# Optimization experiments

Hardware: AMD Instinct MI355X
Metric: run time of the kernel (lower is better)

## Reference

```python
import jax, jax.numpy as jnp
import numpy as np

SHAPE = (4096, 11008)


def setup_inputs() -> dict:
    key = jax.random.key(0)
    k1, k2, k3 = jax.random.split(key, 3)
    x = jax.random.normal(k1, SHAPE, dtype=jnp.float32)
    magnitude = jax.random.uniform(k2, SHAPE, dtype=jnp.float32)  # EMA state (non-negative)
    sparsity = jax.random.uniform(k3, (1,), dtype=jnp.float32)
    mask = jnp.ones(SHAPE, dtype=bool)
    t = 1  # step counter (self.t) as python int
    return {"x": x, "magnitude": magnitude, "sparsity": sparsity, "mask": mask, "t": t}


def reference(x, magnitude, sparsity, mask, t):
    # update_magnitude: EMA of |x| (done under no_grad in torch)
    t_f = jnp.float32(t)
    mag = (t_f * magnitude + jnp.abs(x)) / (t_f + 1.0)
    # prune_and_update_mask: sort-based k-th smallest magnitude threshold
    values = jnp.sort(mag.ravel())
    n = values.shape[0]
    # torch: idx = max(int(sparsity * n - 1), 0)
    idx = jnp.clip(jnp.floor(sparsity * n - 1.0).astype(jnp.int32), 0, n - 1)
    threshold = values[idx]  # shape (1,), broadcasts
    new_mask = mag >= threshold
    # broadcast_mul
    return x * new_mask.astype(x.dtype)
```

## Files before the change

kernel.cpp:

```cpp
#include <hip/hip_runtime.h>
#include <stdint.h>


#define LO_BITS 17
#define NB_HI   (1 << (32 - LO_BITS))
#define NB_LO   (1 << LO_BITS)

__device__ __forceinline__ uint32_t fkey(float f) {
    uint32_t u = __float_as_uint(f);
    return (u & 0x80000000u) ? ~u : (u | 0x80000000u);
}

__device__ __forceinline__ float magf(float x, float g, float tf, float den) {
    return (tf * g + fabsf(x)) / den;
}

__global__ __launch_bounds__(1024) void hist_hi_kernel(
    const float* __restrict__ x, const float* __restrict__ g,
    const int* __restrict__ tptr, uint32_t* __restrict__ hist_hi, int n)
{
    __shared__ uint32_t lh[NB_HI / 2];
    for (int i = threadIdx.x; i < NB_HI / 2; i += blockDim.x) lh[i] = 0;
    __syncthreads();
    const float tf  = (float)tptr[0];
    const float den = tf + 1.0f;
    const int n4 = n >> 2;
    const float4* x4 = (const float4*)x;
    const float4* g4 = (const float4*)g;
    const int gid = blockIdx.x * blockDim.x + threadIdx.x;
    const int stride = gridDim.x * blockDim.x;
    for (int i = gid; i < n4; i += stride) {
        float4 xv = x4[i], gv = g4[i];
        uint32_t b0 = fkey(magf(xv.x, gv.x, tf, den)) >> LO_BITS;
        uint32_t b1 = fkey(magf(xv.y, gv.y, tf, den)) >> LO_BITS;
        uint32_t b2 = fkey(magf(xv.z, gv.z, tf, den)) >> LO_BITS;
        uint32_t b3 = fkey(magf(xv.w, gv.w, tf, den)) >> LO_BITS;
        atomicAdd(&lh[b0 >> 1], 1u << ((b0 & 1) * 16));
        atomicAdd(&lh[b1 >> 1], 1u << ((b1 & 1) * 16));
        atomicAdd(&lh[b2 >> 1], 1u << ((b2 & 1) * 16));
        atomicAdd(&lh[b3 >> 1], 1u << ((b3 & 1) * 16));
    }
    for (int i = (n4 << 2) + gid; i < n; i += stride) {
        uint32_t b = fkey(magf(x[i], g[i], tf, den)) >> LO_BITS;
        atomicAdd(&lh[b >> 1], 1u << ((b & 1) * 16));
    }
    __syncthreads();
    for (int i = threadIdx.x; i < NB_HI / 2; i += blockDim.x) {
        uint32_t v = lh[i];
        uint32_t lo = v & 0xffffu, hi = v >> 16;
        if (lo) atomicAdd(&hist_hi[2 * i],     lo);
        if (hi) atomicAdd(&hist_hi[2 * i + 1], hi);
    }
}

__global__ __launch_bounds__(1024) void scan_kernel(
    const uint32_t* __restrict__ hist, uint32_t* __restrict__ ctl,
    const float* __restrict__ sparsity, int nbins, int phase, int n)
{
    const int tid = threadIdx.x;
    const int bpt = nbins >> 10;
    uint32_t kk;
    if (phase == 0) {
        float s = sparsity[0];
        float v = floorf(s * (float)n - 1.0f);
        long long idx = (long long)v;
        if (idx < 0) idx = 0;
        if (idx > (long long)(n - 1)) idx = n - 1;
        kk = (uint32_t)(idx + 1);
    } else {
        kk = ctl[1];
    }
    const int base = tid * bpt;
    uint32_t s = 0;
    for (int j = 0; j < bpt; ++j) s += hist[base + j];
    __shared__ uint32_t tmp[1024];
    tmp[tid] = s;
    __syncthreads();
    for (int off = 1; off < 1024; off <<= 1) {
        uint32_t v = (tid >= off) ? tmp[tid - off] : 0u;
        __syncthreads();
        tmp[tid] += v;
        __syncthreads();
    }
    const uint32_t incl = tmp[tid];
    const uint32_t excl = incl - s;
    if (excl < kk && incl >= kk) {
        uint32_t running = excl;
        for (int j = 0; j < bpt; ++j) {
            uint32_t c = hist[base + j];
            if (running + c >= kk) {
                uint32_t bin = (uint32_t)(base + j);
                if (phase == 0) { ctl[0] = bin; ctl[1] = kk - running; }
                else            { ctl[2] = (ctl[0] << LO_BITS) | bin; }
                break;
            }
            running += c;
        }
    }
}

__global__ __launch_bounds__(512) void hist_lo_kernel(
    const float* __restrict__ x, const float* __restrict__ g,
    const int* __restrict__ tptr, const uint32_t* __restrict__ ctl,
    uint32_t* __restrict__ hist_lo, int n)
{
    const uint32_t b   = ctl[0];
    const float tf  = (float)tptr[0];
    const float den = tf + 1.0f;
    const int n4 = n >> 2;
    const float4* x4 = (const float4*)x;
    const float4* g4 = (const float4*)g;
    const int gid = blockIdx.x * blockDim.x + threadIdx.x;
    const int stride = gridDim.x * blockDim.x;
    for (int i = gid; i < n4; i += stride) {
        float4 xv = x4[i], gv = g4[i];
        uint32_t k0 = fkey(magf(xv.x, gv.x, tf, den));
        uint32_t k1 = fkey(magf(xv.y, gv.y, tf, den));
        uint32_t k2 = fkey(magf(xv.z, gv.z, tf, den));
        uint32_t k3 = fkey(magf(xv.w, gv.w, tf, den));
        if ((k0 >> LO_BITS) == b) atomicAdd(&hist_lo[k0 & (NB_LO - 1)], 1u);
        if ((k1 >> LO_BITS) == b) atomicAdd(&hist_lo[k1 & (NB_LO - 1)], 1u);
        if ((k2 >> LO_BITS) == b) atomicAdd(&hist_lo[k2 & (NB_LO - 1)], 1u);
        if ((k3 >> LO_BITS) == b) atomicAdd(&hist_lo[k3 & (NB_LO - 1)], 1u);
    }
    for (int i = (n4 << 2) + gid; i < n; i += stride) {
        uint32_t k = fkey(magf(x[i], g[i], tf, den));
        if ((k >> LO_BITS) == b) atomicAdd(&hist_lo[k & (NB_LO - 1)], 1u);
    }
}

__global__ __launch_bounds__(512) void apply_kernel(
    const float* __restrict__ x, const float* __restrict__ g,
    const int* __restrict__ tptr, const uint32_t* __restrict__ ctl,
    float* __restrict__ out, int n)
{
    const uint32_t K = ctl[2];
    const float tf  = (float)tptr[0];
    const float den = tf + 1.0f;
    const int n4 = n >> 2;
    const float4* x4 = (const float4*)x;
    const float4* g4 = (const float4*)g;
    float4* o4 = (float4*)out;
    const int gid = blockIdx.x * blockDim.x + threadIdx.x;
    const int stride = gridDim.x * blockDim.x;
    for (int i = gid; i < n4; i += stride) {
        float4 xv = x4[i], gv = g4[i];
        float4 o;
        o.x = xv.x * ((fkey(magf(xv.x, gv.x, tf, den)) >= K) ? 1.0f : 0.0f);
        o.y = xv.y * ((fkey(magf(xv.y, gv.y, tf, den)) >= K) ? 1.0f : 0.0f);
        o.z = xv.z * ((fkey(magf(xv.z, gv.z, tf, den)) >= K) ? 1.0f : 0.0f);
        o.w = xv.w * ((fkey(magf(xv.w, gv.w, tf, den)) >= K) ? 1.0f : 0.0f);
        o4[i] = o;
    }
    for (int i = (n4 << 2) + gid; i < n; i += stride) {
        out[i] = x[i] * ((fkey(magf(x[i], g[i], tf, den)) >= K) ? 1.0f : 0.0f);
    }
}

extern "C" void kernel_launch(void* const* d_in, const int* in_sizes, int n_in,
                              void* d_out, int out_size, void* d_ws, size_t ws_size,
                              hipStream_t stream)
{
    const float* x  = (const float*)d_in[0];
    const float* g  = (const float*)d_in[1];
    const float* sp = (const float*)d_in[2];
    const int*   t  = (const int*)d_in[4];
    float* out = (float*)d_out;
    const int n = in_sizes[0];

    uint32_t* hist_hi = (uint32_t*)d_ws;
    uint32_t* hist_lo = hist_hi + NB_HI;
    uint32_t* ctl     = hist_lo + NB_LO;

    hipMemsetAsync(d_ws, 0, (size_t)(NB_HI + NB_LO + 3) * sizeof(uint32_t), stream);
    hist_hi_kernel<<<1024, 1024, 0, stream>>>(x, g, t, hist_hi, n);
    scan_kernel<<<1, 1024, 0, stream>>>(hist_hi, ctl, sp, NB_HI, 0, n);
    hist_lo_kernel<<<2048, 512, 0, stream>>>(x, g, t, ctl, hist_lo, n);
    scan_kernel<<<1, 1024, 0, stream>>>(hist_lo, ctl, sp, NB_LO, 1, n);
    apply_kernel<<<2048, 512, 0, stream>>>(x, g, t, ctl, out, n);
}
```

Measured before the change: 679.9 us.

## Parallelize histogram scan into segment sums and unroll streaming kernels with batched loads

Replaces the single-block prefix scan over each histogram with a multi-block segment-sum pass followed by a single block that scans only the chosen segment, so the serial scan over 128K bins is spread across many blocks. The three streaming kernels switch from grid-stride loops to one tile per block, with eight float4 loads per thread issued before any compute to raise memory-level parallelism. This adds two extra kernel launches and a fixed-size grid tied to n, and increases register pressure.

```diff
diff --git a/kernel.cpp b/kernel.cpp
--- a/kernel.cpp
+++ b/kernel.cpp
@@ -5,12 +5,12 @@
 #define LO_BITS 17
 #define NB_HI   (1 << (32 - LO_BITS))
 #define NB_LO   (1 << LO_BITS)
+#define NSEG    64
 
 __device__ __forceinline__ uint32_t fkey(float f) {
     uint32_t u = __float_as_uint(f);
     return (u & 0x80000000u) ? ~u : (u | 0x80000000u);
 }
-
 __device__ __forceinline__ float magf(float x, float g, float tf, float den) {
     return (tf * g + fabsf(x)) / den;
 }
@@ -20,32 +20,43 @@
     const int* __restrict__ tptr, uint32_t* __restrict__ hist_hi, int n)
 {
     __shared__ uint32_t lh[NB_HI / 2];
-    for (int i = threadIdx.x; i < NB_HI / 2; i += blockDim.x) lh[i] = 0;
+    for (int i = threadIdx.x; i < NB_HI / 2; i += 1024) lh[i] = 0;
     __syncthreads();
     const float tf  = (float)tptr[0];
     const float den = tf + 1.0f;
     const int n4 = n >> 2;
     const float4* x4 = (const float4*)x;
     const float4* g4 = (const float4*)g;
-    const int gid = blockIdx.x * blockDim.x + threadIdx.x;
-    const int stride = gridDim.x * blockDim.x;
-    for (int i = gid; i < n4; i += stride) {
-        float4 xv = x4[i], gv = g4[i];
-        uint32_t b0 = fkey(magf(xv.x, gv.x, tf, den)) >> LO_BITS;
-        uint32_t b1 = fkey(magf(xv.y, gv.y, tf, den)) >> LO_BITS;
-        uint32_t b2 = fkey(magf(xv.z, gv.z, tf, den)) >> LO_BITS;
-        uint32_t b3 = fkey(magf(xv.w, gv.w, tf, den)) >> LO_BITS;
-        atomicAdd(&lh[b0 >> 1], 1u << ((b0 & 1) * 16));
-        atomicAdd(&lh[b1 >> 1], 1u << ((b1 & 1) * 16));
-        atomicAdd(&lh[b2 >> 1], 1u << ((b2 & 1) * 16));
-        atomicAdd(&lh[b3 >> 1], 1u << ((b3 & 1) * 16));
-    }
-    for (int i = (n4 << 2) + gid; i < n; i += stride) {
-        uint32_t b = fkey(magf(x[i], g[i], tf, den)) >> LO_BITS;
-        atomicAdd(&lh[b >> 1], 1u << ((b & 1) * 16));
-    }
-    __syncthreads();
-    for (int i = threadIdx.x; i < NB_HI / 2; i += blockDim.x) {
+    const int base = blockIdx.x * 8192 + threadIdx.x;
+
+    float4 xv[8], gv[8];
+    #pragma unroll
+    for (int u = 0; u < 8; ++u) {
+        const int idx = base + u * 1024;
+        if (idx < n4) { xv[u] = x4[idx]; gv[u] = g4[idx]; }
+    }
+    #pragma unroll
+    for (int u = 0; u < 8; ++u) {
+        const int idx = base + u * 1024;
+        if (idx < n4) {
+            uint32_t b0 = fkey(magf(xv[u].x, gv[u].x, tf, den)) >> LO_BITS;
+            uint32_t b1 = fkey(magf(xv[u].y, gv[u].y, tf, den)) >> LO_BITS;
+            uint32_t b2 = fkey(magf(xv[u].z, gv[u].z, tf, den)) >> LO_BITS;
+            uint32_t b3 = fkey(magf(xv[u].w, gv[u].w, tf, den)) >> LO_BITS;
+            atomicAdd(&lh[b0 >> 1], 1u << ((b0 & 1) * 16));
+            atomicAdd(&lh[b1 >> 1], 1u << ((b1 & 1) * 16));
+            atomicAdd(&lh[b2 >> 1], 1u << ((b2 & 1) * 16));
+            atomicAdd(&lh[b3 >> 1], 1u << ((b3 & 1) * 16));
+        }
+    }
+    if (blockIdx.x == 0) {
+        for (int i = (n4 << 2) + threadIdx.x; i < n; i += 1024) {
+            uint32_t b = fkey(magf(x[i], g[i], tf, den)) >> LO_BITS;
+            atomicAdd(&lh[b >> 1], 1u << ((b & 1) * 16));
+        }
+    }
+    __syncthreads();
+    for (int i = threadIdx.x; i < NB_HI / 2; i += 1024) {
         uint32_t v = lh[i];
         uint32_t lo = v & 0xffffu, hi = v >> 16;
         if (lo) atomicAdd(&hist_hi[2 * i],     lo);
@@ -53,53 +64,95 @@
     }
 }
 
-__global__ __launch_bounds__(1024) void scan_kernel(
-    const uint32_t* __restrict__ hist, uint32_t* __restrict__ ctl,
-    const float* __restrict__ sparsity, int nbins, int phase, int n)
-{
+__global__ __launch_bounds__(256) void seg_kernel(
+    const uint32_t* __restrict__ hist, uint32_t* __restrict__ segsum, int bps)
+{
+    __shared__ uint32_t red[256];
+    const int base = blockIdx.x * bps;
+    uint32_t s = 0;
+    for (int j = threadIdx.x; j < bps; j += 256) s += hist[base + j];
+    red[threadIdx.x] = s;
+    __syncthreads();
+    for (int off = 128; off > 0; off >>= 1) {
+        if (threadIdx.x < off) red[threadIdx.x] += red[threadIdx.x + off];
+        __syncthreads();
+    }
+    if (threadIdx.x == 0) segsum[blockIdx.x] = red[0];
+}
+
+__global__ __launch_bounds__(1024) void find_kernel(
+    const uint32_t* __restrict__ hist, const uint32_t* __restrict__ segsum,
+    uint32_t* __restrict__ ctl, const float* __restrict__ sparsity,
+    int nbins, int phase, int n)
+{
+    const int bps = nbins / NSEG;
+    __shared__ uint32_t sseg[NSEG];
+    __shared__ uint32_t bins[2048];
+    __shared__ uint32_t scanbuf[1024];
+    __shared__ uint32_t skk, sseg_id;
     const int tid = threadIdx.x;
-    const int bpt = nbins >> 10;
-    uint32_t kk;
-    if (phase == 0) {
-        float s = sparsity[0];
-        float v = floorf(s * (float)n - 1.0f);
-        long long idx = (long long)v;
-        if (idx < 0) idx = 0;
-        if (idx > (long long)(n - 1)) idx = n - 1;
-        kk = (uint32_t)(idx + 1);
-    } else {
-        kk = ctl[1];
-    }
-    const int base = tid * bpt;
+    if (tid < NSEG) sseg[tid] = segsum[tid];
+    __syncthreads();
+    if (tid == 0) {
+        uint32_t kk;
+        if (phase == 0) {
+            float s = sparsity[0];
+            float v = floorf(s * (float)n - 1.0f);
+            long long idx = (long long)v;
+            if (idx < 0) idx = 0;
+            if (idx > (long long)(n - 1)) idx = n - 1;
+            kk = (uint32_t)(idx + 1);
+        } else {
+            kk = ctl[1];
+        }
+        uint32_t run = 0; uint32_t seg = NSEG - 1;
+        for (int j = 0; j < NSEG; ++j) {
+            if (run + sseg[j] >= kk) { seg = (uint32_t)j; break; }
+            run += sseg[j];
+        }
+        skk = kk - run;
+        sseg_id = seg;
+    }
+    __syncthreads();
+    const uint32_t kk = skk;
+    const int seg = (int)sseg_id;
+    for (int j = tid; j < bps; j += 1024) bins[j] = hist[seg * bps + j];
+    __syncthreads();
+    const int c = (bps + 1023) >> 10;
     uint32_t s = 0;
-    for (int j = 0; j < bpt; ++j) s += hist[base + j];
-    __shared__ uint32_t tmp[1024];
-    tmp[tid] = s;
+    for (int j = 0; j < c; ++j) {
+        int b0 = tid * c + j;
+        if (b0 < bps) s += bins[b0];
+    }
+    scanbuf[tid] = s;
     __syncthreads();
     for (int off = 1; off < 1024; off <<= 1) {
-        uint32_t v = (tid >= off) ? tmp[tid - off] : 0u;
+        uint32_t v = (tid >= off) ? scanbuf[tid - off] : 0u;
         __syncthreads();
-        tmp[tid] += v;
+        scanbuf[tid] += v;
         __syncthreads();
     }
-    const uint32_t incl = tmp[tid];
+    const uint32_t incl = scanbuf[tid];
     const uint32_t excl = incl - s;
     if (excl < kk && incl >= kk) {
-        uint32_t running = excl;
-        for (int j = 0; j < bpt; ++j) {
-            uint32_t c = hist[base + j];
-            if (running + c >= kk) {
-                uint32_t bin = (uint32_t)(base + j);
-                if (phase == 0) { ctl[0] = bin; ctl[1] = kk - running; }
-                else            { ctl[2] = (ctl[0] << LO_BITS) | bin; }
-                break;
+        uint32_t run = excl;
+        for (int j = 0; j < c; ++j) {
+            int b0 = tid * c + j;
+            if (b0 < bps) {
+                uint32_t cc = bins[b0];
+                if (run + cc >= kk) {
+                    uint32_t bin = (uint32_t)(seg * bps + b0);
+                    if (phase == 0) { ctl[0] = bin; ctl[1] = kk - run; }
+                    else            { ctl[2] = (ctl[0] << LO_BITS) | bin; }
+                    break;
+                }
+                run += cc;
             }
-            running += c;
-        }
-    }
-}
-
-__global__ __launch_bounds__(512) void hist_lo_kernel(
+        }
+    }
+}
+
+__global__ __launch_bounds__(256) void hist_lo_kernel(
     const float* __restrict__ x, const float* __restrict__ g,
     const int* __restrict__ tptr, const uint32_t* __restrict__ ctl,
     uint32_t* __restrict__ hist_lo, int n)
@@ -110,26 +163,37 @@
     const int n4 = n >> 2;
     const float4* x4 = (const float4*)x;
     const float4* g4 = (const float4*)g;
-    const int gid = blockIdx.x * blockDim.x + threadIdx.x;
-    const int stride = gridDim.x * blockDim.x;
-    for (int i = gid; i < n4; i += stride) {
-        float4 xv = x4[i], gv = g4[i];
-        uint32_t k0 = fkey(magf(xv.x, gv.x, tf, den));
-        uint32_t k1 = fkey(magf(xv.y, gv.y, tf, den));
-        uint32_t k2 = fkey(magf(xv.z, gv.z, tf, den));
-        uint32_t k3 = fkey(magf(xv.w, gv.w, tf, den));
-        if ((k0 >> LO_BITS) == b) atomicAdd(&hist_lo[k0 & (NB_LO - 1)], 1u);
-        if ((k1 >> LO_BITS) == b) atomicAdd(&hist_lo[k1 & (NB_LO - 1)], 1u);
-        if ((k2 >> LO_BITS) == b) atomicAdd(&hist_lo[k2 & (NB_LO - 1)], 1u);
-        if ((k3 >> LO_BITS) == b) atomicAdd(&hist_lo[k3 & (NB_LO - 1)], 1u);
-    }
-    for (int i = (n4 << 2) + gid; i < n; i += stride) {
-        uint32_t k = fkey(magf(x[i], g[i], tf, den));
-        if ((k >> LO_BITS) == b) atomicAdd(&hist_lo[k & (NB_LO - 1)], 1u);
-    }
-}
-
-__global__ __launch_bounds__(512) void apply_kernel(
+    const int base = blockIdx.x * 2048 + threadIdx.x;
+
+    float4 xv[8], gv[8];
+    #pragma unroll
+    for (int u = 0; u < 8; ++u) {
+        const int idx = base + u * 256;
+        if (idx < n4) { xv[u] = x4[idx]; gv[u] = g4[idx]; }
+    }
+    #pragma unroll
+    for (int u = 0; u < 8; ++u) {
+        const int idx = base + u * 256;
+        if (idx < n4) {
+            uint32_t k0 = fkey(magf(xv[u].x, gv[u].x, tf, den));
+            uint32_t k1 = fkey(magf(xv[u].y, gv[u].y, tf, den));
+            uint32_t k2 = fkey(magf(xv[u].z, gv[u].z, tf, den));
+            uint32_t k3 = fkey(magf(xv[u].w, gv[u].w, tf, den));
+            if ((k0 >> LO_BITS) == b) atomicAdd(&hist_lo[k0 & (NB_LO - 1)], 1u);
+            if ((k1 >> LO_BITS) == b) atomicAdd(&hist_lo[k1 & (NB_LO - 1)], 1u);
+            if ((k2 >> LO_BITS) == b) atomicAdd(&hist_lo[k2 & (NB_LO - 1)], 1u);
+            if ((k3 >> LO_BITS) == b) atomicAdd(&hist_lo[k3 & (NB_LO - 1)], 1u);
+        }
+    }
+    if (blockIdx.x == 0) {
+        for (int i = (n4 << 2) + threadIdx.x; i < n; i += 256) {
+            uint32_t k = fkey(magf(x[i], g[i], tf, den));
+            if ((k >> LO_BITS) == b) atomicAdd(&hist_lo[k & (NB_LO - 1)], 1u);
+        }
+    }
+}
+
+__global__ __launch_bounds__(256) void apply_kernel(
     const float* __restrict__ x, const float* __restrict__ g,
     const int* __restrict__ tptr, const uint32_t* __restrict__ ctl,
     float* __restrict__ out, int n)
@@ -141,19 +205,30 @@
     const float4* x4 = (const float4*)x;
     const float4* g4 = (const float4*)g;
     float4* o4 = (float4*)out;
-    const int gid = blockIdx.x * blockDim.x + threadIdx.x;
-    const int stride = gridDim.x * blockDim.x;
-    for (int i = gid; i < n4; i += stride) {
-        float4 xv = x4[i], gv = g4[i];
-        float4 o;
-        o.x = xv.x * ((fkey(magf(xv.x, gv.x, tf, den)) >= K) ? 1.0f : 0.0f);
-        o.y = xv.y * ((fkey(magf(xv.y, gv.y, tf, den)) >= K) ? 1.0f : 0.0f);
-        o.z = xv.z * ((fkey(magf(xv.z, gv.z, tf, den)) >= K) ? 1.0f : 0.0f);
-        o.w = xv.w * ((fkey(magf(xv.w, gv.w, tf, den)) >= K) ? 1.0f : 0.0f);
-        o4[i] = o;
-    }
-    for (int i = (n4 << 2) + gid; i < n; i += stride) {
-        out[i] = x[i] * ((fkey(magf(x[i], g[i], tf, den)) >= K) ? 1.0f : 0.0f);
+    const int base = blockIdx.x * 2048 + threadIdx.x;
+
+    float4 xv[8], gv[8];
+    #pragma unroll
+    for (int u = 0; u < 8; ++u) {
+        const int idx = base + u * 256;
+        if (idx < n4) { xv[u] = x4[idx]; gv[u] = g4[idx]; }
+    }
+    #pragma unroll
+    for (int u = 0; u < 8; ++u) {
+        const int idx = base + u * 256;
+        if (idx < n4) {
+            float4 o;
+            o.x = xv[u].x * ((fkey(magf(xv[u].x, gv[u].x, tf, den)) >= K) ? 1.0f : 0.0f);
+            o.y = xv[u].y * ((fkey(magf(xv[u].y, gv[u].y, tf, den)) >= K) ? 1.0f : 0.0f);
+            o.z = xv[u].z * ((fkey(magf(xv[u].z, gv[u].z, tf, den)) >= K) ? 1.0f : 0.0f);
+            o.w = xv[u].w * ((fkey(magf(xv[u].w, gv[u].w, tf, den)) >= K) ? 1.0f : 0.0f);
+            o4[idx] = o;
+        }
+    }
+    if (blockIdx.x == 0) {
+        for (int i = (n4 << 2) + threadIdx.x; i < n; i += 256) {
+            out[i] = x[i] * ((fkey(magf(x[i], g[i], tf, den)) >= K) ? 1.0f : 0.0f);
+        }
     }
 }
 
@@ -166,16 +241,24 @@
     const float* sp = (const float*)d_in[2];
     const int*   t  = (const int*)d_in[4];
     float* out = (float*)d_out;
-    const int n = in_sizes[0];
+    const int n  = in_sizes[0];
+    const int n4 = n >> 2;
 
     uint32_t* hist_hi = (uint32_t*)d_ws;
     uint32_t* hist_lo = hist_hi + NB_HI;
-    uint32_t* ctl     = hist_lo + NB_LO;
-
-    hipMemsetAsync(d_ws, 0, (size_t)(NB_HI + NB_LO + 3) * sizeof(uint32_t), stream);
-    hist_hi_kernel<<<1024, 1024, 0, stream>>>(x, g, t, hist_hi, n);
-    scan_kernel<<<1, 1024, 0, stream>>>(hist_hi, ctl, sp, NB_HI, 0, n);
-    hist_lo_kernel<<<2048, 512, 0, stream>>>(x, g, t, ctl, hist_lo, n);
-    scan_kernel<<<1, 1024, 0, stream>>>(hist_lo, ctl, sp, NB_LO, 1, n);
-    apply_kernel<<<2048, 512, 0, stream>>>(x, g, t, ctl, out, n);
-}
+    uint32_t* segsum  = hist_lo + NB_LO;
+    uint32_t* ctl     = segsum + NSEG;
+
+    hipMemsetAsync(d_ws, 0, (size_t)(NB_HI + NB_LO + NSEG + 3) * sizeof(uint32_t), stream);
+
+    const int g_hi = (n4 + 8191) / 8192;
+    const int g_lo = (n4 + 2047) / 2048;
+
+    hist_hi_kernel<<<g_hi, 1024, 0, stream>>>(x, g, t, hist_hi, n);
+    seg_kernel<<<NSEG, 256, 0, stream>>>(hist_hi, segsum, NB_HI / NSEG);
+    find_kernel<<<1, 1024, 0, stream>>>(hist_hi, segsum, ctl, sp, NB_HI, 0, n);
+    hist_lo_kernel<<<g_lo, 256, 0, stream>>>(x, g, t, ctl, hist_lo, n);
+    seg_kernel<<<NSEG, 256, 0, stream>>>(hist_lo, segsum, NB_LO / NSEG);
+    find_kernel<<<1, 1024, 0, stream>>>(hist_lo, segsum, ctl, sp, NB_LO, 1, n);
+    apply_kernel<<<g_lo, 256, 0, stream>>>(x, g, t, ctl, out, n);
+}
```

Result: faster. 652.0 us (-4.1%).
